# Optimization experiments

Measured on AMD Instinct MI355X. Metric: run time of the kernel, lower is better.

Reference implementation:

```python
import jax, jax.numpy as jnp
import numpy as np

H = 16          # num_heads
R = 4           # query compression ratio
WIN = 128       # sliding window size
NEG = -1e9      # finite mask value (safe softmax grads)


def setup_inputs() -> dict:
    key = jax.random.key(0)
    k0, k1, k2, k3, k4 = jax.random.split(key, 5)
    B, S, D = 4, 4096, 2048
    inputs = jax.random.normal(k0, (B, S, D), jnp.float32)
    attention_mask = jnp.ones((B, S), jnp.int32)
    s = 0.02
    Wq = jax.random.normal(k1, (D, D), jnp.float32) * s
    Wk = jax.random.normal(k2, (D, D), jnp.float32) * s
    Wv = jax.random.normal(k3, (D, D), jnp.float32) * s
    Wo = jax.random.normal(k4, (D, D), jnp.float32) * s
    return {"inputs": inputs, "attention_mask": attention_mask,
            "Wq": Wq, "Wk": Wk, "Wv": Wv, "Wo": Wo}


def _forward(inputs, attention_mask, Wq, Wk, Wv, Wo):
    B, S, D = inputs.shape
    dh = D // H
    scale = 1.0 / np.sqrt(dh).astype(np.float32)
    Cs = (S + R - 1) // R            # compressed query length (S % R == 0 here)
    win = min(WIN, S)
    ws = max(0, S - win)             # window start

    # Q projection -> [B,H,S,dh] -> compress groups of R by mean -> [B,H,Cs,dh]
    q = jnp.einsum('bsd,od->bso', inputs, Wq)
    q = q.reshape(B, S, H, dh).transpose(0, 2, 1, 3)
    qc = q.reshape(B, H, Cs, R, dh).mean(axis=3)

    # K/V only over the recent window
    wx = inputs[:, ws:ws + win, :]
    k = jnp.einsum('bsd,od->bso', wx, Wk).reshape(B, win, H, dh).transpose(0, 2, 1, 3)
    v = jnp.einsum('bsd,od->bso', wx, Wv).reshape(B, win, H, dh).transpose(0, 2, 1, 3)

    scores = jnp.einsum('bhqd,bhkd->bhqk', qc, k) * scale

    # causal mask: each compressed query sits at position (i+1)*R-1
    qpos = (jnp.arange(Cs) + 1) * R - 1                     # [Cs]
    wpos = ws + jnp.arange(win)
    causal = wpos[None, :] <= qpos[:, None]
    qbw = qpos < ws                                         # queries fully before window
    causal = causal.at[:, 0].set(causal[:, 0] | qbw)
    pad_ok = (attention_mask[:, ws:ws + win] != 0)
    full = causal[None, None, :, :] & pad_ok[:, None, None, :]

    scores = jnp.where(full, scores, NEG)
    weights = jax.nn.softmax(scores, axis=-1)
    out = jnp.einsum('bhqk,bhkd->bhqd', weights, v)         # [B,H,Cs,dh]
    out = out.transpose(0, 2, 1, 3).reshape(B, Cs, D)
    out = jnp.einsum('bsd,od->bso', out, Wo)

    if Cs != S:  # linear interpolation back to seq_len (align_corners=False)
        out = jax.image.resize(out, (B, S, D), method='linear')
    return out


def reference(inputs, attention_mask, Wq, Wk, Wv, Wo):
    return _forward(inputs, attention_mask, Wq, Wk, Wv, Wo)
```

## Files before the change

kernel.cpp:

```cpp
#include <hip/hip_runtime.h>
#include <hip/hip_bf16.h>


typedef __attribute__((ext_vector_type(8))) short short8;
typedef __attribute__((ext_vector_type(4))) float f32x4;

#define QP_SLICE  (128 * 2048)
#define KV_SLICE  (512 * 2048)
#define YO_STRIDE (132 * 2048)

__device__ __forceinline__ unsigned short f2bf(float f){
  unsigned int x = __float_as_uint(f);
  return (unsigned short)((x + 0x7fffu + ((x >> 16) & 1u)) >> 16);
}
__device__ __forceinline__ float bf2f(unsigned short u){
  return __uint_as_float(((unsigned int)u) << 16);
}
__device__ __forceinline__ float bflo(unsigned int u){ return __uint_as_float(u << 16); }
__device__ __forceinline__ float bfhi(unsigned int u){ return __uint_as_float(u & 0xffff0000u); }
__device__ __forceinline__ unsigned int pk2(float lo, float hi){
  return ((unsigned int)f2bf(hi) << 16) | (unsigned int)f2bf(lo);
}
__device__ __forceinline__ short8 cvt8(float4 x, float4 y){
  union { unsigned int u[4]; short8 s; } r;
  r.u[0] = pk2(x.x, x.y); r.u[1] = pk2(x.z, x.w);
  r.u[2] = pk2(y.x, y.y); r.u[3] = pk2(y.z, y.w);
  return r.s;
}

__global__ __launch_bounds__(256) void prep_kernel(
    const float* __restrict__ inp,
    const float* __restrict__ Wq, const float* __restrict__ Wk,
    const float* __restrict__ Wv, const float* __restrict__ Wo,
    unsigned short* __restrict__ Wb,
    unsigned short* __restrict__ Awx, unsigned short* __restrict__ Aq)
{
  const int bx = blockIdx.x;
  if (bx < 8192){
    const int idx = bx * 256 + threadIdx.x;
    const int w = idx >> 19;
    const int sub = idx & 524287;
    const float* src = (w == 0) ? Wq : (w == 1) ? Wk : (w == 2) ? Wv : Wo;
    const float* p = src + (size_t)sub * 8;
    *(short8*)&Wb[(size_t)w * 4194304 + (size_t)sub * 8] =
        cvt8(*(const float4*)p, *(const float4*)(p + 4));
  } else if (bx < 8704){
    const int idx = (bx - 8192) * 256 + threadIdx.x;
    const int b = idx >> 15;
    const int j = (idx >> 8) & 127;
    const int d8 = (idx & 255) * 8;
    const float* p = inp + ((size_t)b * 4096 + 3968 + j) * 2048 + d8;
    *(short8*)&Awx[((size_t)b * 128 + j) * 2048 + d8] =
        cvt8(*(const float4*)p, *(const float4*)(p + 4));
  } else {
    const int idx = (bx - 8704) * 256 + threadIdx.x;
    const int b = idx >> 13;
    const int c = (idx >> 8) & 31;
    const int d8 = (idx & 255) * 8;
    const float* p = inp + ((size_t)b * 4096 + 3968 + 4 * c) * 2048 + d8;
    float4 x0 = *(const float4*)(p);
    float4 x1 = *(const float4*)(p + 2048);
    float4 x2 = *(const float4*)(p + 4096);
    float4 x3 = *(const float4*)(p + 6144);
    float4 y0 = *(const float4*)(p + 4);
    float4 y1 = *(const float4*)(p + 2052);
    float4 y2 = *(const float4*)(p + 4100);
    float4 y3 = *(const float4*)(p + 6148);
    float4 xm, ym;
    xm.x = 0.25f * (x0.x + x1.x + x2.x + x3.x);
    xm.y = 0.25f * (x0.y + x1.y + x2.y + x3.y);
    xm.z = 0.25f * (x0.z + x1.z + x2.z + x3.z);
    xm.w = 0.25f * (x0.w + x1.w + x2.w + x3.w);
    ym.x = 0.25f * (y0.x + y1.x + y2.x + y3.x);
    ym.y = 0.25f * (y0.y + y1.y + y2.y + y3.y);
    ym.z = 0.25f * (y0.z + y1.z + y2.z + y3.z);
    ym.w = 0.25f * (y0.w + y1.w + y2.w + y3.w);
    *(short8*)&Aq[((size_t)b * 32 + c) * 2048 + d8] = cvt8(xm, ym);
  }
}

__device__ __forceinline__ void stage_tile(
    const unsigned short* __restrict__ A, const unsigned short* __restrict__ W,
    int row0, int n0, int kt,
    unsigned short* As, unsigned short* Bs, int wid, int lane)
{
  const int r  = lane >> 3;
  const int ug = ((lane & 7) ^ r) * 8;
  #pragma unroll
  for (int i = 0; i < 4; ++i){
    const int c = wid * 4 + i;
    __builtin_amdgcn_global_load_lds(
        (const __attribute__((address_space(1))) void*)(A + (size_t)(row0 + c * 8 + r) * 2048 + kt + ug),
        (__attribute__((address_space(3))) void*)(As + c * 512),
        16, 0, 0);
    __builtin_amdgcn_global_load_lds(
        (const __attribute__((address_space(1))) void*)(W + (size_t)(n0 + c * 8 + r) * 2048 + kt + ug),
        (__attribute__((address_space(3))) void*)(Bs + c * 512),
        16, 0, 0);
  }
}

template<bool OUT_BF16>
__device__ __forceinline__ void gemm_body(
    const unsigned short* __restrict__ A, const unsigned short* __restrict__ W,
    unsigned short* __restrict__ Cb, float* __restrict__ Cf,
    int M, int row0, int n0, int kbase, int nsteps,
    unsigned short* L)
{
  const int tid  = threadIdx.x;
  const int lane = tid & 63;
  const int wid  = tid >> 6;
  const int wr = wid >> 1, wc = wid & 1;

  f32x4 acc[4][4] = {};

  stage_tile(A, W, row0, n0, kbase, L, L + 8192, wid, lane);
  int cur = 0;

  for (int t = 0; t < nsteps; ++t){
    __syncthreads();
    const int nxt = cur ^ 1;
    if (t + 1 < nsteps)
      stage_tile(A, W, row0, n0, kbase + (t + 1) * 64,
                 L + nxt * 16384, L + nxt * 16384 + 8192, wid, lane);
    const unsigned short* As = L + cur * 16384;
    const unsigned short* Bs = As + 8192;
    #pragma unroll
    for (int ks = 0; ks < 2; ++ks){
      short8 av[4], bv[4];
      const int unit = ks * 4 + (lane >> 4);
      #pragma unroll
      for (int f = 0; f < 4; ++f){
        const int row = wr * 64 + f * 16 + (lane & 15);
        av[f] = *(const short8*)&As[row * 64 + ((unit ^ (row & 7)) * 8)];
      }
      #pragma unroll
      for (int n = 0; n < 4; ++n){
        const int row = wc * 64 + n * 16 + (lane & 15);
        bv[n] = *(const short8*)&Bs[row * 64 + ((unit ^ (row & 7)) * 8)];
      }
      #pragma unroll
      for (int f = 0; f < 4; ++f)
        #pragma unroll
        for (int n = 0; n < 4; ++n)
          acc[f][n] = __builtin_amdgcn_mfma_f32_16x16x32_bf16(av[f], bv[n], acc[f][n], 0, 0, 0);
    }
    cur = nxt;
  }

  #pragma unroll
  for (int f = 0; f < 4; ++f){
    #pragma unroll
    for (int n = 0; n < 4; ++n){
      const int col = n0 + wc * 64 + n * 16 + (lane & 15);
      #pragma unroll
      for (int r = 0; r < 4; ++r){
        const int row = row0 + wr * 64 + f * 16 + (lane >> 4) * 4 + r;
        if (row < M){
          if (OUT_BF16) Cb[(size_t)row * 2048 + col] = f2bf(acc[f][n][r]);
          else          Cf[(size_t)row * 2048 + col] = acc[f][n][r];
        }
      }
    }
  }
}

__global__ __launch_bounds__(256, 2) void qkv_kernel(
    const unsigned short* __restrict__ Aq, const unsigned short* __restrict__ Awx,
    const unsigned short* __restrict__ Wb,
    unsigned short* __restrict__ Qp, unsigned short* __restrict__ Kp,
    unsigned short* __restrict__ Vp)
{
  __shared__ __align__(16) unsigned short L[32768];
  const int nt = blockIdx.x, gy = blockIdx.y;
  if (gy < 2){
    gemm_body<true>(Aq, Wb, Qp + gy * QP_SLICE, nullptr,
                    128, 0, nt * 128, gy * 1024, 16, L);
  } else if (gy < 10){
    const int idx = gy - 2, mt = idx >> 1, ksp = idx & 1;
    gemm_body<true>(Awx, Wb + 4194304, Kp + ksp * KV_SLICE, nullptr,
                    512, mt * 128, nt * 128, ksp * 1024, 16, L);
  } else {
    const int idx = gy - 10, mt = idx >> 1, ksp = idx & 1;
    gemm_body<true>(Awx, Wb + 8388608, Vp + ksp * KV_SLICE, nullptr,
                    512, mt * 128, nt * 128, ksp * 1024, 16, L);
  }
}

__global__ __launch_bounds__(256, 2) void o_kernel(
    const unsigned short* __restrict__ Ao, const unsigned short* __restrict__ Wb,
    float* __restrict__ Yop)
{
  __shared__ __align__(16) unsigned short L[32768];
  gemm_body<false>(Ao, Wb + 12582912, nullptr, Yop + (size_t)blockIdx.z * YO_STRIDE,
                   132, blockIdx.y * 128, blockIdx.x * 128, blockIdx.z * 512, 8, L);
}

__global__ __launch_bounds__(256) void attn_kernel(
    const unsigned short* __restrict__ Qp, const unsigned short* __restrict__ Kp,
    const unsigned short* __restrict__ Vp, const int* __restrict__ amask,
    unsigned short* __restrict__ Ao)
{
  const int b = blockIdx.x >> 4;
  const int h = blockIdx.x & 15;
  __shared__ float Qs[32][129];
  __shared__ unsigned int Ks[128][65];
  __shared__ unsigned int Vs[128][65];
  __shared__ float Wt[32][132];
  __shared__ float msk[128];
  const int tid = threadIdx.x;

  for (int i = tid; i < 32 * 128; i += 256){
    int cq = i >> 7, d = i & 127;
    size_t off = (size_t)(b * 32 + cq) * 2048 + h * 128 + d;
    Qs[cq][d] = bf2f(Qp[off]) + bf2f(Qp[off + QP_SLICE]);
  }
  for (int i = tid; i < 128 * 64; i += 256){
    int j = i >> 6, du = i & 63;
    size_t off = (size_t)(b * 128 + j) * 2048 + h * 128 + du * 2;
    unsigned int k0 = *(const unsigned int*)(Kp + off);
    unsigned int k1 = *(const unsigned int*)(Kp + off + KV_SLICE);
    unsigned int v0 = *(const unsigned int*)(Vp + off);
    unsigned int v1 = *(const unsigned int*)(Vp + off + KV_SLICE);
    Ks[j][du] = pk2(bflo(k0) + bflo(k1), bfhi(k0) + bfhi(k1));
    Vs[j][du] = pk2(bflo(v0) + bflo(v1), bfhi(v0) + bfhi(v1));
  }
  if (tid < 128){
    msk[tid] = (amask[b * 4096 + 3968 + tid] != 0) ? 1.f : 0.f;
    size_t off = (size_t)(b * 128) * 2048 + h * 128 + tid;
    Ao[(size_t)(b * 33) * 2048 + h * 128 + tid] =
        f2bf(bf2f(Vp[off]) + bf2f(Vp[off + KV_SLICE]));
  }
  __syncthreads();

  const int cq = tid >> 3, jg = tid & 7;
  const int jmax = 4 * cq + 3;
  const float scale = 0.088388347648318447f;

  float s[16];
  {
    float sacc[16];
    #pragma unroll
    for (int jj = 0; jj < 16; ++jj) sacc[jj] = 0.f;
    for (int du = 0; du < 64; ++du){
      float q0 = Qs[cq][2 * du], q1 = Qs[cq][2 * du + 1];
      #pragma unroll
      for (int jj = 0; jj < 16; ++jj){
        unsigned int u = Ks[jg * 16 + jj][du];
        sacc[jj] += q0 * bflo(u) + q1 * bfhi(u);
      }
    }
    #pragma unroll
    for (int jj = 0; jj < 16; ++jj){
      int j = jg * 16 + jj;
      bool ok = (j <= jmax) && (msk[j] > 0.5f);
      s[jj] = ok ? sacc[jj] * scale : -1e9f;
    }
  }
  float m = s[0];
  #pragma unroll
  for (int jj = 1; jj < 16; ++jj) m = fmaxf(m, s[jj]);
  #pragma unroll
  for (int off = 1; off < 8; off <<= 1) m = fmaxf(m, __shfl_xor(m, off, 8));
  float sum = 0.f;
  #pragma unroll
  for (int jj = 0; jj < 16; ++jj){ s[jj] = expf(s[jj] - m); sum += s[jj]; }
  #pragma unroll
  for (int off = 1; off < 8; off <<= 1) sum += __shfl_xor(sum, off, 8);
  const float inv = 1.f / sum;
  #pragma unroll
  for (int jj = 0; jj < 16; ++jj) Wt[cq][jg * 16 + jj] = s[jj] * inv;
  __syncthreads();

  const int dg = tid & 7;
  float o[16];
  #pragma unroll
  for (int e = 0; e < 16; ++e) o[e] = 0.f;
  for (int j = 0; j < 128; ++j){
    float w = Wt[cq][j];
    #pragma unroll
    for (int du = 0; du < 8; ++du){
      unsigned int u = Vs[j][dg * 8 + du];
      o[2 * du]     += w * bflo(u);
      o[2 * du + 1] += w * bfhi(u);
    }
  }
  unsigned short* dst = Ao + (size_t)(b * 33 + 1 + cq) * 2048 + h * 128 + dg * 16;
  #pragma unroll
  for (int e = 0; e < 16; ++e) dst[e] = f2bf(o[e]);
}

__global__ __launch_bounds__(256) void resize_kernel(
    const float* __restrict__ Yop, float* __restrict__ out)
{
  const int rowid = blockIdx.x;
  const int b = rowid >> 12;
  const int i = rowid & 4095;
  float c  = i * 0.25f - 0.375f;
  float fl = floorf(c);
  int   j0 = (int)fl;
  float f  = c - fl;
  int   j1 = j0 + 1;
  j0 = max(0, min(j0, 1023));
  j1 = max(0, min(j1, 1023));
  const int ri0 = b * 33 + (j0 <= 991 ? 0 : j0 - 991);
  const int ri1 = b * 33 + (j1 <= 991 ? 0 : j1 - 991);
  const float* r0 = Yop + (size_t)ri0 * 2048;
  const float* r1 = Yop + (size_t)ri1 * 2048;
  float* op = out + (size_t)rowid * 2048;
  const int t = threadIdx.x;
  const bool same = (ri0 == ri1);
  #pragma unroll
  for (int q = 0; q < 2; ++q){
    int d = q * 1024 + t * 4;
    float4 a0 = *(const float4*)(r0 + d);
    float4 a1 = *(const float4*)(r0 + d + YO_STRIDE);
    float4 a2 = *(const float4*)(r0 + d + 2 * YO_STRIDE);
    float4 a3 = *(const float4*)(r0 + d + 3 * YO_STRIDE);
    float4 a;
    a.x = a0.x + a1.x + a2.x + a3.x;
    a.y = a0.y + a1.y + a2.y + a3.y;
    a.z = a0.z + a1.z + a2.z + a3.z;
    a.w = a0.w + a1.w + a2.w + a3.w;
    float4 o = a;
    if (!same){
      float4 b0 = *(const float4*)(r1 + d);
      float4 b1 = *(const float4*)(r1 + d + YO_STRIDE);
      float4 b2 = *(const float4*)(r1 + d + 2 * YO_STRIDE);
      float4 b3 = *(const float4*)(r1 + d + 3 * YO_STRIDE);
      float4 bb;
      bb.x = b0.x + b1.x + b2.x + b3.x;
      bb.y = b0.y + b1.y + b2.y + b3.y;
      bb.z = b0.z + b1.z + b2.z + b3.z;
      bb.w = b0.w + b1.w + b2.w + b3.w;
      o.x = a.x + f * (bb.x - a.x);
      o.y = a.y + f * (bb.y - a.y);
      o.z = a.z + f * (bb.z - a.z);
      o.w = a.w + f * (bb.w - a.w);
    }
    *(float4*)(op + d) = o;
  }
}

extern "C" void kernel_launch(void* const* d_in, const int* in_sizes, int n_in,
                              void* d_out, int out_size, void* d_ws, size_t ws_size,
                              hipStream_t stream)
{
  const float* inp   = (const float*)d_in[0];
  const int*   amask = (const int*)d_in[1];
  const float* Wq = (const float*)d_in[2];
  const float* Wk = (const float*)d_in[3];
  const float* Wv = (const float*)d_in[4];
  const float* Wo = (const float*)d_in[5];
  float* out = (float*)d_out;

  char* ws = (char*)d_ws;
  unsigned short* Wb  = (unsigned short*)(ws);
  unsigned short* Aq  = (unsigned short*)(ws + 33554432);
  unsigned short* Awx = (unsigned short*)(ws + 34078720);
  unsigned short* Qp  = (unsigned short*)(ws + 36175872);
  unsigned short* Kp  = (unsigned short*)(ws + 37224448);
  unsigned short* Vp  = (unsigned short*)(ws + 41418752);
  unsigned short* Ao  = (unsigned short*)(ws + 45613056);
  float*          Yop = (float*)(ws + 46661632);

  prep_kernel<<<8832, 256, 0, stream>>>(inp, Wq, Wk, Wv, Wo, Wb, Awx, Aq);
  qkv_kernel<<<dim3(16, 18), 256, 0, stream>>>(Aq, Awx, Wb, Qp, Kp, Vp);
  attn_kernel<<<64, 256, 0, stream>>>(Qp, Kp, Vp, amask, Ao);
  o_kernel<<<dim3(16, 2, 4), 256, 0, stream>>>(Ao, Wb, Yop);
  resize_kernel<<<16384, 256, 0, stream>>>(Yop, out);
}
```

Before: 111.3 us.

## Fuse fp32-to-bf16 weight conversion into GEMM B-tile staging

Drops the separate pass that converted all four fp32 weight matrices to bf16 in workspace. The GEMMs now load fp32 weight rows into registers, convert them to bf16 and write them swizzled into LDS, with register prefetch of the next tile overlapping the MFMA loop. This removes a full write and re-read of the bf16 weights, at the cost of twice the global bytes per weight tile read inside the GEMM and VALU conversion work in the inner loop.

```diff
diff --git a/kernel.cpp b/kernel.cpp
--- a/kernel.cpp
+++ b/kernel.cpp
@@ -30,22 +30,11 @@
 
 __global__ __launch_bounds__(256) void prep_kernel(
     const float* __restrict__ inp,
-    const float* __restrict__ Wq, const float* __restrict__ Wk,
-    const float* __restrict__ Wv, const float* __restrict__ Wo,
-    unsigned short* __restrict__ Wb,
     unsigned short* __restrict__ Awx, unsigned short* __restrict__ Aq)
 {
   const int bx = blockIdx.x;
-  if (bx < 8192){
+  if (bx < 512){
     const int idx = bx * 256 + threadIdx.x;
-    const int w = idx >> 19;
-    const int sub = idx & 524287;
-    const float* src = (w == 0) ? Wq : (w == 1) ? Wk : (w == 2) ? Wv : Wo;
-    const float* p = src + (size_t)sub * 8;
-    *(short8*)&Wb[(size_t)w * 4194304 + (size_t)sub * 8] =
-        cvt8(*(const float4*)p, *(const float4*)(p + 4));
-  } else if (bx < 8704){
-    const int idx = (bx - 8192) * 256 + threadIdx.x;
     const int b = idx >> 15;
     const int j = (idx >> 8) & 127;
     const int d8 = (idx & 255) * 8;
@@ -53,7 +42,7 @@
     *(short8*)&Awx[((size_t)b * 128 + j) * 2048 + d8] =
         cvt8(*(const float4*)p, *(const float4*)(p + 4));
   } else {
-    const int idx = (bx - 8704) * 256 + threadIdx.x;
+    const int idx = (bx - 512) * 256 + threadIdx.x;
     const int b = idx >> 13;
     const int c = (idx >> 8) & 31;
     const int d8 = (idx & 255) * 8;
@@ -79,10 +68,9 @@
   }
 }
 
-__device__ __forceinline__ void stage_tile(
-    const unsigned short* __restrict__ A, const unsigned short* __restrict__ W,
-    int row0, int n0, int kt,
-    unsigned short* As, unsigned short* Bs, int wid, int lane)
+__device__ __forceinline__ void stage_a(
+    const unsigned short* __restrict__ A, int row0, int kt,
+    unsigned short* As, int wid, int lane)
 {
   const int r  = lane >> 3;
   const int ug = ((lane & 7) ^ r) * 8;
@@ -93,16 +81,12 @@
         (const __attribute__((address_space(1))) void*)(A + (size_t)(row0 + c * 8 + r) * 2048 + kt + ug),
         (__attribute__((address_space(3))) void*)(As + c * 512),
         16, 0, 0);
-    __builtin_amdgcn_global_load_lds(
-        (const __attribute__((address_space(1))) void*)(W + (size_t)(n0 + c * 8 + r) * 2048 + kt + ug),
-        (__attribute__((address_space(3))) void*)(Bs + c * 512),
-        16, 0, 0);
   }
 }
 
 template<bool OUT_BF16>
 __device__ __forceinline__ void gemm_body(
-    const unsigned short* __restrict__ A, const unsigned short* __restrict__ W,
+    const unsigned short* __restrict__ A, const float* __restrict__ W,
     unsigned short* __restrict__ Cb, float* __restrict__ Cf,
     int M, int row0, int n0, int kbase, int nsteps,
     unsigned short* L)
@@ -112,17 +96,36 @@
   const int wid  = tid >> 6;
   const int wr = wid >> 1, wc = wid & 1;
 
+  const int brow = tid & 127;
+  const int bhalf = tid >> 7;
+  const float* Wrow = W + (size_t)(n0 + brow) * 2048 + bhalf * 32;
+
   f32x4 acc[4][4] = {};
-
-  stage_tile(A, W, row0, n0, kbase, L, L + 8192, wid, lane);
+  float4 pb[8];
+
+  stage_a(A, row0, kbase, L, wid, lane);
+  #pragma unroll
+  for (int q = 0; q < 8; ++q) pb[q] = *(const float4*)(Wrow + kbase + q * 4);
+  {
+    unsigned short* Bs = L + 8192;
+    #pragma unroll
+    for (int u4 = 0; u4 < 4; ++u4){
+      const int unit = bhalf * 4 + u4;
+      *(short8*)&Bs[brow * 64 + ((unit ^ (brow & 7)) * 8)] = cvt8(pb[2 * u4], pb[2 * u4 + 1]);
+    }
+  }
+  __syncthreads();
   int cur = 0;
 
   for (int t = 0; t < nsteps; ++t){
-    __syncthreads();
     const int nxt = cur ^ 1;
-    if (t + 1 < nsteps)
-      stage_tile(A, W, row0, n0, kbase + (t + 1) * 64,
-                 L + nxt * 16384, L + nxt * 16384 + 8192, wid, lane);
+    const bool pf = (t + 1) < nsteps;
+    if (pf){
+      const int kt = kbase + (t + 1) * 64;
+      stage_a(A, row0, kt, L + nxt * 16384, wid, lane);
+      #pragma unroll
+      for (int q = 0; q < 8; ++q) pb[q] = *(const float4*)(Wrow + kt + q * 4);
+    }
     const unsigned short* As = L + cur * 16384;
     const unsigned short* Bs = As + 8192;
     #pragma unroll
@@ -145,6 +148,15 @@
         for (int n = 0; n < 4; ++n)
           acc[f][n] = __builtin_amdgcn_mfma_f32_16x16x32_bf16(av[f], bv[n], acc[f][n], 0, 0, 0);
     }
+    if (pf){
+      unsigned short* Bn = L + nxt * 16384 + 8192;
+      #pragma unroll
+      for (int u4 = 0; u4 < 4; ++u4){
+        const int unit = bhalf * 4 + u4;
+        *(short8*)&Bn[brow * 64 + ((unit ^ (brow & 7)) * 8)] = cvt8(pb[2 * u4], pb[2 * u4 + 1]);
+      }
+    }
+    __syncthreads();
     cur = nxt;
   }
 
@@ -167,32 +179,32 @@
 
 __global__ __launch_bounds__(256, 2) void qkv_kernel(
     const unsigned short* __restrict__ Aq, const unsigned short* __restrict__ Awx,
-    const unsigned short* __restrict__ Wb,
+    const float* __restrict__ Wq, const float* __restrict__ Wk, const float* __restrict__ Wv,
     unsigned short* __restrict__ Qp, unsigned short* __restrict__ Kp,
     unsigned short* __restrict__ Vp)
 {
   __shared__ __align__(16) unsigned short L[32768];
   const int nt = blockIdx.x, gy = blockIdx.y;
   if (gy < 2){
-    gemm_body<true>(Aq, Wb, Qp + gy * QP_SLICE, nullptr,
+    gemm_body<true>(Aq, Wq, Qp + gy * QP_SLICE, nullptr,
                     128, 0, nt * 128, gy * 1024, 16, L);
   } else if (gy < 10){
     const int idx = gy - 2, mt = idx >> 1, ksp = idx & 1;
-    gemm_body<true>(Awx, Wb + 4194304, Kp + ksp * KV_SLICE, nullptr,
+    gemm_body<true>(Awx, Wk, Kp + ksp * KV_SLICE, nullptr,
                     512, mt * 128, nt * 128, ksp * 1024, 16, L);
   } else {
     const int idx = gy - 10, mt = idx >> 1, ksp = idx & 1;
-    gemm_body<true>(Awx, Wb + 8388608, Vp + ksp * KV_SLICE, nullptr,
+    gemm_body<true>(Awx, Wv, Vp + ksp * KV_SLICE, nullptr,
                     512, mt * 128, nt * 128, ksp * 1024, 16, L);
   }
 }
 
 __global__ __launch_bounds__(256, 2) void o_kernel(
-    const unsigned short* __restrict__ Ao, const unsigned short* __restrict__ Wb,
+    const unsigned short* __restrict__ Ao, const float* __restrict__ Wo,
     float* __restrict__ Yop)
 {
   __shared__ __align__(16) unsigned short L[32768];
-  gemm_body<false>(Ao, Wb + 12582912, nullptr, Yop + (size_t)blockIdx.z * YO_STRIDE,
+  gemm_body<false>(Ao, Wo, nullptr, Yop + (size_t)blockIdx.z * YO_STRIDE,
                    132, blockIdx.y * 128, blockIdx.x * 128, blockIdx.z * 512, 8, L);
 }
 
@@ -355,18 +367,17 @@
   float* out = (float*)d_out;
 
   char* ws = (char*)d_ws;
-  unsigned short* Wb  = (unsigned short*)(ws);
-  unsigned short* Aq  = (unsigned short*)(ws + 33554432);
-  unsigned short* Awx = (unsigned short*)(ws + 34078720);
-  unsigned short* Qp  = (unsigned short*)(ws + 36175872);
-  unsigned short* Kp  = (unsigned short*)(ws + 37224448);
-  unsigned short* Vp  = (unsigned short*)(ws + 41418752);
-  unsigned short* Ao  = (unsigned short*)(ws + 45613056);
-  float*          Yop = (float*)(ws + 46661632);
-
-  prep_kernel<<<8832, 256, 0, stream>>>(inp, Wq, Wk, Wv, Wo, Wb, Awx, Aq);
-  qkv_kernel<<<dim3(16, 18), 256, 0, stream>>>(Aq, Awx, Wb, Qp, Kp, Vp);
+  unsigned short* Aq  = (unsigned short*)(ws);
+  unsigned short* Awx = (unsigned short*)(ws + 524288);
+  unsigned short* Qp  = (unsigned short*)(ws + 2621440);
+  unsigned short* Kp  = (unsigned short*)(ws + 3670016);
+  unsigned short* Vp  = (unsigned short*)(ws + 7864320);
+  unsigned short* Ao  = (unsigned short*)(ws + 12058624);
+  float*          Yop = (float*)(ws + 13107200);
+
+  prep_kernel<<<640, 256, 0, stream>>>(inp, Awx, Aq);
+  qkv_kernel<<<dim3(16, 18), 256, 0, stream>>>(Aq, Awx, Wq, Wk, Wv, Qp, Kp, Vp);
   attn_kernel<<<64, 256, 0, stream>>>(Qp, Kp, Vp, amask, Ao);
-  o_kernel<<<dim3(16, 2, 4), 256, 0, stream>>>(Ao, Wb, Yop);
+  o_kernel<<<dim3(16, 2, 4), 256, 0, stream>>>(Ao, Wo, Yop);
   resize_kernel<<<16384, 256, 0, stream>>>(Yop, out);
 }
```

Result: slower. 137.5 us (+23.5%).
